# Kernel optimization log

Measured on AMD Instinct MI355X. Metric: run time of the kernel, lower is better.

Reference implementation:

```python
import jax, jax.numpy as jnp
import numpy as np

H = 1024        # hidden_size
NH = 16         # num heads
HD = H // NH    # head dim = 64
B, S = 2, 2048


def _linear_params(key, fan_in, fan_out):
    k1, k2 = jax.random.split(key)
    bound = 1.0 / np.sqrt(fan_in)
    w = jax.random.uniform(k1, (fan_in, fan_out), jnp.float32, -bound, bound)
    b = jax.random.uniform(k2, (fan_out,), jnp.float32, -bound, bound)
    return w, b


def setup_inputs() -> dict:
    key = jax.random.key(0)
    ks = jax.random.split(key, 10)
    hidden_states = jax.random.normal(ks[0], (B, S, H), jnp.float32)
    topic_states = jax.random.normal(ks[1], (B, H), jnp.float32)
    attention_mask = jnp.zeros((B, 1, 1, S), jnp.float32)
    Wq, bq = _linear_params(ks[2], H, H)
    Wk, bk = _linear_params(ks[3], H, H)
    Wv, bv = _linear_params(ks[4], H, H)
    Wtp, btp = _linear_params(ks[5], H, H)
    Wta, bta = _linear_params(ks[6], H, H)
    Wd, bd = _linear_params(ks[7], H, H)
    ln_g = jnp.ones((H,), jnp.float32)
    ln_b = jnp.zeros((H,), jnp.float32)
    return {
        "hidden_states": hidden_states, "topic_states": topic_states,
        "attention_mask": attention_mask,
        "Wq": Wq, "bq": bq, "Wk": Wk, "bk": bk, "Wv": Wv, "bv": bv,
        "Wtp": Wtp, "btp": btp, "Wta": Wta, "bta": bta,
        "Wd": Wd, "bd": bd, "ln_g": ln_g, "ln_b": ln_b,
    }


def reference(hidden_states, topic_states, attention_mask,
              Wq, bq, Wk, bk, Wv, bv, Wtp, btp, Wta, bta, Wd, bd, ln_g, ln_b):
    # topic gating: two linears on [B,H], broadcast over seq
    topic_proj = topic_states @ Wtp + btp
    topic_att = topic_proj @ Wta + bta                     # [B,H]
    gate = jax.nn.sigmoid(topic_att)[:, None, :]           # [B,1,H]

    q = hidden_states @ Wq + bq                            # [B,S,H]
    k = (hidden_states @ Wk + bk) * gate                   # sigmoid-gated keys
    v = hidden_states @ Wv + bv

    def split_heads(x):  # [B,S,H] -> [B,NH,S,HD]
        return x.reshape(B, S, NH, HD).transpose(0, 2, 1, 3)

    qh, kh, vh = split_heads(q), split_heads(k), split_heads(v)

    scores = jnp.einsum('bhqd,bhkd->bhqk', qh, kh) / np.sqrt(HD).astype(np.float32)
    scores = scores + attention_mask                       # additive mask
    probs = jax.nn.softmax(scores, axis=-1)                # dropout = identity (eval)
    ctx = jnp.einsum('bhqk,bhkd->bhqd', probs, vh)
    ctx = ctx.transpose(0, 2, 1, 3).reshape(B, S, H)

    out = ctx @ Wd + bd                                    # dense + (eval) dropout
    x = out + hidden_states                                # residual
    mu = jnp.mean(x, axis=-1, keepdims=True)
    var = jnp.mean(jnp.square(x - mu), axis=-1, keepdims=True)
    return (x - mu) * jax.lax.rsqrt(var + 1e-5) * ln_g + ln_b
```

## Files before the change

### kernel.cpp

```cpp
#include <hip/hip_runtime.h>

typedef unsigned short u16;
typedef unsigned int   u32;
typedef __attribute__((ext_vector_type(4)))  float f32x4;
typedef __attribute__((ext_vector_type(16))) float f32x16;
typedef __attribute__((ext_vector_type(8)))  __bf16 bf16x8;
typedef __attribute__((ext_vector_type(8)))  u16  u16x8;
typedef __attribute__((ext_vector_type(4)))  u16  u16x4;

#define HDIM 1024
#define SEQ  2048
#define NB   2
#define MROWS 4096
#define QSCALE 0.18033688011111793f
#define LOG2E  1.4426950408889634f
#define TOPK 64
#define TOPC 16

__device__ __forceinline__ u16 f2bf(float f) {
  u32 u = __float_as_uint(f);
  u32 r = u + 0x7FFFu + ((u >> 16) & 1u);
  return (u16)(r >> 16);
}

__device__ __forceinline__ u32 pkbf(float a, float b) {
  union { __bf16 h[2]; u32 w; } u;
  u.h[0] = (__bf16)a; u.h[1] = (__bf16)b;
  return u.w;
}

__device__ __forceinline__ void gload_lds16(const void* gp, void* lp) {
  __builtin_amdgcn_global_load_lds(
      (const __attribute__((address_space(1))) void*)gp,
      (__attribute__((address_space(3))) void*)lp, 16, 0, 0);
}

__global__ void wt_bf16_kernel(const float* __restrict__ w0, const float* __restrict__ w1,
                               const float* __restrict__ w2, const float* __restrict__ w3,
                               u16* __restrict__ out) {
  const float* W = (blockIdx.z == 0) ? w0 : (blockIdx.z == 1) ? w1 : (blockIdx.z == 2) ? w2 : w3;
  u16* Wt = out + (size_t)blockIdx.z * HDIM * HDIM;
  __shared__ float t[32][33];
  const int k0 = blockIdx.x * 32, n0 = blockIdx.y * 32;
  const int tx = threadIdx.x, ty = threadIdx.y;
#pragma unroll
  for (int j = 0; j < 32; j += 8)
    t[ty + j][tx] = W[(size_t)(k0 + ty + j) * HDIM + n0 + tx];
  __syncthreads();
#pragma unroll
  for (int j = 0; j < 32; j += 8)
    Wt[(size_t)(n0 + ty + j) * HDIM + k0 + tx] = f2bf(t[tx][ty + j]);
}

__global__ void cvt_bf16_kernel(const float* __restrict__ in, u16* __restrict__ out) {
  const size_t i = (size_t)blockIdx.x * 256 + threadIdx.x;
  f32x4 v = *(const f32x4*)(in + i * 4);
  u16x4 o;
#pragma unroll
  for (int e = 0; e < 4; ++e) o[e] = f2bf(v[e]);
  *(u16x4*)(out + i * 4) = o;
}

__global__ void topic_partial_kernel(const float* __restrict__ in, const float* __restrict__ W,
                                     float* __restrict__ part) {
  const int c = blockIdx.x;
  const int b = blockIdx.y;
  const int t = threadIdx.x;
  const float* inb = in + b * HDIM + c * TOPK;
  f32x4 acc = {};
#pragma unroll 8
  for (int k = 0; k < TOPK; ++k) {
    const f32x4 w4 = *(const f32x4*)(W + (size_t)(c * TOPK + k) * HDIM + t * 4);
    acc += inb[k] * w4;
  }
  *(f32x4*)(part + ((size_t)(b * TOPC + c)) * HDIM + t * 4) = acc;
}

__global__ void topic_reduce_kernel(const float* __restrict__ part, const float* __restrict__ bias,
                                    float* __restrict__ out, int sigmoid_mode) {
  const int b = blockIdx.y;
  const int n = blockIdx.x * 256 + threadIdx.x;
  float s = bias[n];
#pragma unroll
  for (int c = 0; c < TOPC; ++c) s += part[((size_t)(b * TOPC + c)) * HDIM + n];
  out[b * HDIM + n] = sigmoid_mode ? (1.f / (1.f + __expf(-s))) : s;
}

template <int MODE>
__global__ __launch_bounds__(256, 2)
void gemm_kernel(const u16* __restrict__ A, const u16* __restrict__ Wt,
                 const float* __restrict__ b0, const float* __restrict__ b1,
                 const float* __restrict__ b2, const float* __restrict__ gate,
                 const float* __restrict__ resid,
                 u16* __restrict__ outb, float* __restrict__ outf) {
  const int n0 = blockIdx.x * 128;
  const int m0 = blockIdx.y * 128;
  const int z = blockIdx.z;
  const u16* W = Wt + (size_t)z * (HDIM * HDIM);
  const float* bias = (MODE == 0) ? (z == 0 ? b0 : (z == 1 ? b1 : b2)) : b0;

  __shared__ __align__(16) u16 Alds[128 * 64];
  __shared__ __align__(16) u16 Blds[128 * 64];

  const int tid = threadIdx.x;
  const int lane = tid & 63;
  const int w = tid >> 6;
  const int wm = w >> 1, wn = w & 1;
  const int srow = tid >> 3, sslot = tid & 7;

  f32x4 acc[4][4] = {};

  for (int k0 = 0; k0 < HDIM; k0 += 64) {
    __syncthreads();
#pragma unroll
    for (int j = 0; j < 4; ++j) {
      const int row = j * 32 + srow;
      const int gs = (sslot ^ (row & 7)) * 8;
      gload_lds16(A + (size_t)(m0 + row) * HDIM + k0 + gs, Alds + j * 2048 + w * 512);
      gload_lds16(W + (size_t)(n0 + row) * HDIM + k0 + gs, Blds + j * 2048 + w * 512);
    }
    __syncthreads();
#pragma unroll
    for (int kk = 0; kk < 2; ++kk) {
      const int slot = ((((kk << 2) + (lane >> 4)) ^ (lane & 7)) << 3);
      bf16x8 af[4], bfr[4];
#pragma unroll
      for (int i = 0; i < 4; ++i) {
        af[i]  = *(const bf16x8*)(&Alds[(wm * 64 + i * 16 + (lane & 15)) * 64 + slot]);
        bfr[i] = *(const bf16x8*)(&Blds[(wn * 64 + i * 16 + (lane & 15)) * 64 + slot]);
      }
#pragma unroll
      for (int i = 0; i < 4; ++i)
#pragma unroll
        for (int jn = 0; jn < 4; ++jn)
          acc[i][jn] = __builtin_amdgcn_mfma_f32_16x16x32_bf16(af[i], bfr[jn], acc[i][jn], 0, 0, 0);
    }
  }

  const int rbase = (lane >> 4) << 2;
#pragma unroll
  for (int i = 0; i < 4; ++i) {
#pragma unroll
    for (int jn = 0; jn < 4; ++jn) {
      const int n = n0 + wn * 64 + jn * 16 + (lane & 15);
      const float bv = bias[n];
#pragma unroll
      for (int r = 0; r < 4; ++r) {
        const int m = m0 + wm * 64 + i * 16 + rbase + r;
        float v = acc[i][jn][r] + bv;
        if (MODE == 0) {
          if (z == 0) v *= QSCALE;
          if (z == 1) v *= gate[(m >> 11) * HDIM + n];
          outb[(size_t)z * MROWS * HDIM + (size_t)m * HDIM + n] = f2bf(v);
        } else {
          v += resid[(size_t)m * HDIM + n];
          outf[(size_t)m * HDIM + n] = v;
        }
      }
    }
  }
}

__global__ void vtrans_kernel(const u16* __restrict__ v, u16* __restrict__ vt) {
  const int s0 = blockIdx.x * 64, h = blockIdx.y, b = blockIdx.z;
  __shared__ u16 T[64][66];
  const int tid = threadIdx.x;
  const int r = tid >> 3, c8 = (tid & 7) * 8;
#pragma unroll
  for (int p = 0; p < 2; ++p) {
    const int srow = p * 32 + r;
    const u16x8 val = *(const u16x8*)(v + (size_t)(b * SEQ + s0 + srow) * HDIM + h * 64 + c8);
#pragma unroll
    for (int e = 0; e < 8; ++e) T[srow][c8 + e] = val[e];
  }
  __syncthreads();
#pragma unroll
  for (int p = 0; p < 2; ++p) {
    const int drow = p * 32 + r;
    u16x8 o;
#pragma unroll
    for (int e = 0; e < 8; ++e) o[e] = T[c8 + e][drow];
    *(u16x8*)(vt + (size_t)((b * 16 + h) * 64 + drow) * SEQ + s0 + c8) = o;
  }
}

__global__ __launch_bounds__(256, 2)
void attn_kernel(const u16* __restrict__ Q, const u16* __restrict__ K,
                 const u16* __restrict__ Vt, const float* __restrict__ mask,
                 u16* __restrict__ O) {
  const int q0 = blockIdx.x * 128;
  const int h = blockIdx.y;
  const int b = blockIdx.z;
  const size_t base = ((size_t)b * SEQ) * HDIM + h * 64;
  const size_t vtbase = (size_t)((b * 16 + h) * 64) * SEQ;
  const int tid = threadIdx.x, lane = tid & 63, w = tid >> 6;
  const int hh = lane >> 5;
  const int ql = lane & 31;
  const int NT = SEQ / 64;

  __shared__ __align__(16) u16 Kss[2][64 * 64];
  __shared__ __align__(16) u16 Vts[2][64 * 64];

  bf16x8 Qf[4];
  {
    const u16* qp = Q + base + (size_t)(q0 + w * 32 + ql) * HDIM;
#pragma unroll
    for (int ds = 0; ds < 4; ++ds)
      Qf[ds] = *(const bf16x8*)(qp + ds * 16 + hh * 8);
  }

  const int l3 = lane >> 3, l7 = lane & 7;
  const u16* ksrc0 = K + base + (size_t)(w * 8 + l3) * HDIM + ((l7 ^ l3) << 3);
  const u16* ksrc1 = K + base + (size_t)((4 + w) * 8 + l3) * HDIM + ((l7 ^ l3) << 3);
  const u16* vsrc0 = Vt + vtbase + (size_t)(w * 16 + l3) * SEQ + (((l7 ^ l3 ^ (w * 2)) & 7) << 3);
  const u16* vsrc1 = Vt + vtbase + (size_t)(w * 16 + 8 + l3) * SEQ + (((l7 ^ l3 ^ (w * 2 + 1)) & 7) << 3);

  const u16* kaddr[4];
#pragma unroll
  for (int ds = 0; ds < 4; ++ds)
    kaddr[ds] = &Kss[0][ql * 64 + (((ds * 2 + hh) ^ (ql & 7)) << 3)];
  const u16* vaddr[2][4];
#pragma unroll
  for (int dt = 0; dt < 2; ++dt) {
    const int d = dt * 32 + ql;
    const int sw = (d & 7) ^ ((d >> 3) & 7);
#pragma unroll
    for (int c = 0; c < 4; ++c)
      vaddr[dt][c] = &Vts[0][d * 64 + (((c * 2 + hh) ^ sw) << 3)];
  }

  float m_run = -1e30f, l_run = 0.f;
  f32x16 accA = {}, accB = {};

  auto STAGE = [&](int ncur, int t1) {
    const size_t ko = (size_t)(t1 * 64) * HDIM;
    const int vo = t1 * 64;
    gload_lds16(ksrc0 + ko, &Kss[ncur][w * 512]);
    gload_lds16(ksrc1 + ko, &Kss[ncur][(4 + w) * 512]);
    gload_lds16(vsrc0 + vo, &Vts[ncur][w * 1024]);
    gload_lds16(vsrc1 + vo, &Vts[ncur][w * 1024 + 512]);
  };

  STAGE(0, 0);
  __syncthreads();

  auto BODY = [&](int t, const int cur) {
    if (t + 1 < NT) STAGE(cur ^ 1, t + 1);
    const int kvt0 = t * 64;
#pragma unroll
    for (int kvb = 0; kvb < 2; ++kvb) {
      f32x16 sv = {};
#pragma unroll
      for (int ds = 0; ds < 4; ++ds) {
        const bf16x8 kf = *(const bf16x8*)(kaddr[ds] + cur * 4096 + kvb * 2048);
        sv = __builtin_amdgcn_mfma_f32_32x32x16_bf16(kf, Qf[ds], sv, 0, 0, 0);
      }
      f32x4 m4[4];
      {
        const float* mrow = mask + (size_t)b * SEQ + kvt0 + kvb * 32 + hh * 4;
#pragma unroll
        for (int g = 0; g < 4; ++g) m4[g] = *(const f32x4*)(mrow + g * 8);
      }
      f32x16 s_;
#pragma unroll
      for (int j = 0; j < 16; ++j) s_[j] = fmaf(m4[j >> 2][j & 3], LOG2E, sv[j]);

      float mx0 = fmaxf(fmaxf(s_[0], s_[1]), fmaxf(s_[2], s_[3]));
      float mx1 = fmaxf(fmaxf(s_[4], s_[5]), fmaxf(s_[6], s_[7]));
      float mx2 = fmaxf(fmaxf(s_[8], s_[9]), fmaxf(s_[10], s_[11]));
      float mx3 = fmaxf(fmaxf(s_[12], s_[13]), fmaxf(s_[14], s_[15]));
      float mx = fmaxf(fmaxf(mx0, mx1), fmaxf(mx2, mx3));
      mx = fmaxf(mx, __shfl_xor(mx, 32));

      if (!__all(mx <= m_run + 8.f)) {
        const float mnew = fmaxf(m_run, mx);
        const float corr = __builtin_amdgcn_exp2f(m_run - mnew);
        m_run = mnew;
        l_run *= corr;
#pragma unroll
        for (int j = 0; j < 16; ++j) {
          const float cj = __shfl(corr, (j & 3) + 8 * (j >> 2) + 4 * hh);
          accA[j] *= cj; accB[j] *= cj;
        }
      }

      f32x16 p_;
#pragma unroll
      for (int j = 0; j < 16; ++j) p_[j] = __builtin_amdgcn_exp2f(s_[j] - m_run);
      {
        float r0 = (p_[0] + p_[1]) + (p_[2] + p_[3]);
        float r1 = (p_[4] + p_[5]) + (p_[6] + p_[7]);
        float r2 = (p_[8] + p_[9]) + (p_[10] + p_[11]);
        float r3 = (p_[12] + p_[13]) + (p_[14] + p_[15]);
        float rs = (r0 + r1) + (r2 + r3);
        rs += __shfl_xor(rs, 32);
        l_run += rs;
      }

#pragma unroll
      for (int s2 = 0; s2 < 2; ++s2) {
        const u32 a0 = pkbf(p_[s2 * 8 + 0], p_[s2 * 8 + 1]);
        const u32 a1 = pkbf(p_[s2 * 8 + 2], p_[s2 * 8 + 3]);
        const u32 b0v = pkbf(p_[s2 * 8 + 4], p_[s2 * 8 + 5]);
        const u32 b1v = pkbf(p_[s2 * 8 + 6], p_[s2 * 8 + 7]);
        const u32 sd0 = hh ? a0 : b0v, sd1 = hh ? a1 : b1v;
        const u32 r0 = (u32)__shfl_xor((int)sd0, 32);
        const u32 r1 = (u32)__shfl_xor((int)sd1, 32);
        union { u32 u[4]; bf16x8 v; } pu;
        pu.u[0] = hh ? r0 : a0;  pu.u[1] = hh ? r1 : a1;
        pu.u[2] = hh ? b0v : r0; pu.u[3] = hh ? b1v : r1;
        const int c = kvb * 2 + s2;
        const bf16x8 vf0 = *(const bf16x8*)(vaddr[0][c] + cur * 4096);
        const bf16x8 vf1 = *(const bf16x8*)(vaddr[1][c] + cur * 4096);
        accA = __builtin_amdgcn_mfma_f32_32x32x16_bf16(pu.v, vf0, accA, 0, 0, 0);
        accB = __builtin_amdgcn_mfma_f32_32x32x16_bf16(pu.v, vf1, accB, 0, 0, 0);
      }
    }
    __syncthreads();
  };

  for (int tt = 0; tt < NT; tt += 2) {
    BODY(tt, 0);
    BODY(tt + 1, 1);
  }

  const float linv = 1.f / l_run;
#pragma unroll
  for (int j = 0; j < 16; ++j) {
    const int rq = (j & 3) + 8 * (j >> 2) + 4 * hh;
    const float lj = __shfl(linv, rq);
    const size_t orow = base + (size_t)(q0 + w * 32 + rq) * HDIM;
    O[orow + ql]      = f2bf(accA[j] * lj);
    O[orow + 32 + ql] = f2bf(accB[j] * lj);
  }
}

__global__ void ln_kernel(const float* __restrict__ x, const float* __restrict__ g,
                          const float* __restrict__ bb, float* __restrict__ out) {
  const int row = blockIdx.x;
  const int tid = threadIdx.x;
  const f32x4 v = *(const f32x4*)(x + (size_t)row * HDIM + tid * 4);
  float s = v[0] + v[1] + v[2] + v[3];
  float s2 = v[0] * v[0] + v[1] * v[1] + v[2] * v[2] + v[3] * v[3];
#pragma unroll
  for (int o = 1; o < 64; o <<= 1) { s += __shfl_xor(s, o); s2 += __shfl_xor(s2, o); }
  __shared__ float rs[4], rs2[4];
  if ((tid & 63) == 0) { rs[tid >> 6] = s; rs2[tid >> 6] = s2; }
  __syncthreads();
  s = rs[0] + rs[1] + rs[2] + rs[3];
  s2 = rs2[0] + rs2[1] + rs2[2] + rs2[3];
  const float mu = s * (1.f / HDIM);
  const float var = s2 * (1.f / HDIM) - mu * mu;
  const float inv = rsqrtf(var + 1e-5f);
  f32x4 o4;
#pragma unroll
  for (int e = 0; e < 4; ++e) {
    const int c = tid * 4 + e;
    o4[e] = (v[e] - mu) * inv * g[c] + bb[c];
  }
  *(f32x4*)(out + (size_t)row * HDIM + tid * 4) = o4;
}

extern "C" void kernel_launch(void* const* d_in, const int* in_sizes, int n_in,
                              void* d_out, int out_size, void* d_ws, size_t ws_size,
                              hipStream_t stream) {
  const float* hidden = (const float*)d_in[0];
  const float* topic  = (const float*)d_in[1];
  const float* mask   = (const float*)d_in[2];
  const float* Wq  = (const float*)d_in[3];  const float* bq  = (const float*)d_in[4];
  const float* Wk  = (const float*)d_in[5];  const float* bk  = (const float*)d_in[6];
  const float* Wv  = (const float*)d_in[7];  const float* bv  = (const float*)d_in[8];
  const float* Wtp = (const float*)d_in[9];  const float* btp = (const float*)d_in[10];
  const float* Wta = (const float*)d_in[11]; const float* bta = (const float*)d_in[12];
  const float* Wd  = (const float*)d_in[13]; const float* bd  = (const float*)d_in[14];
  const float* lng = (const float*)d_in[15]; const float* lnb = (const float*)d_in[16];
  float* out = (float*)d_out;

  char* ws = (char*)d_ws;
  u16* hs_bf  = (u16*)(ws);
  u16* WtAll  = (u16*)(ws + (size_t)(8u << 20));
  u16* qkv    = (u16*)(ws + (size_t)(16u << 20));
  u16* ctx    = (u16*)(ws + (size_t)(40u << 20));
  u16* VtG    = (u16*)(ws + (size_t)(48u << 20));
  float* xbuf = (float*)(ws + (size_t)(16u << 20));
  float* tproj = (float*)(ws + (size_t)(64u << 20));
  float* tgate = (float*)(ws + (size_t)(64u << 20) + 8192);
  float* tpart = (float*)(ws + (size_t)(16u << 20));

  wt_bf16_kernel<<<dim3(32, 32, 4), dim3(32, 8), 0, stream>>>(Wq, Wk, Wv, Wd, WtAll);
  cvt_bf16_kernel<<<4096, 256, 0, stream>>>(hidden, hs_bf);
  topic_partial_kernel<<<dim3(TOPC, NB), 256, 0, stream>>>(topic, Wtp, tpart);
  topic_reduce_kernel<<<dim3(4, NB), 256, 0, stream>>>(tpart, btp, tproj, 0);
  topic_partial_kernel<<<dim3(TOPC, NB), 256, 0, stream>>>(tproj, Wta, tpart);
  topic_reduce_kernel<<<dim3(4, NB), 256, 0, stream>>>(tpart, bta, tgate, 1);
  gemm_kernel<0><<<dim3(8, 32, 3), 256, 0, stream>>>(hs_bf, WtAll, bq, bk, bv, tgate,
                                                     nullptr, qkv, nullptr);
  vtrans_kernel<<<dim3(32, 16, NB), 256, 0, stream>>>(qkv + 2 * (size_t)MROWS * HDIM, VtG);
  attn_kernel<<<dim3(16, 16, NB), 256, 0, stream>>>(qkv, qkv + (size_t)MROWS * HDIM,
                                                    VtG, mask, ctx);
  gemm_kernel<1><<<dim3(8, 32, 1), 256, 0, stream>>>(ctx, WtAll + 3 * (size_t)HDIM * HDIM,
                                                     bd, nullptr, nullptr, nullptr, hidden,
                                                     nullptr, xbuf);
  ln_kernel<<<4096, 256, 0, stream>>>(xbuf, lng, lnb, out);
}
```

Measured before the change: 166.3 us.

## Load K and V tiles directly from global into registers, dropping LDS staging

Replaces the double-buffered shared-memory staging of K and V tiles (global-to-LDS loads plus barriers) with direct per-lane global loads into registers. K fragments for the next tile are software-prefetched into a second register set while the current tile is computed. This removes LDS traffic and the per-tile __syncthreads. In exchange, each of the four waves now loads K/V redundantly from global/L2, and the extra fragment registers raise VGPR pressure, which may hurt occupancy.

New measurement: 224.4 us. 1.35x slower.

```diff
diff --git a/kernel.cpp b/kernel.cpp
--- a/kernel.cpp
+++ b/kernel.cpp
@@ -192,15 +192,11 @@
   const int h = blockIdx.y;
   const int b = blockIdx.z;
   const size_t base = ((size_t)b * SEQ) * HDIM + h * 64;
-  const size_t vtbase = (size_t)((b * 16 + h) * 64) * SEQ;
   const int tid = threadIdx.x, lane = tid & 63, w = tid >> 6;
   const int hh = lane >> 5;
   const int ql = lane & 31;
   const int NT = SEQ / 64;
 
-  __shared__ __align__(16) u16 Kss[2][64 * 64];
-  __shared__ __align__(16) u16 Vts[2][64 * 64];
-
   bf16x8 Qf[4];
   {
     const u16* qp = Q + base + (size_t)(q0 + w * 32 + ql) * HDIM;
@@ -209,55 +205,48 @@
       Qf[ds] = *(const bf16x8*)(qp + ds * 16 + hh * 8);
   }
 
-  const int l3 = lane >> 3, l7 = lane & 7;
-  const u16* ksrc0 = K + base + (size_t)(w * 8 + l3) * HDIM + ((l7 ^ l3) << 3);
-  const u16* ksrc1 = K + base + (size_t)((4 + w) * 8 + l3) * HDIM + ((l7 ^ l3) << 3);
-  const u16* vsrc0 = Vt + vtbase + (size_t)(w * 16 + l3) * SEQ + (((l7 ^ l3 ^ (w * 2)) & 7) << 3);
-  const u16* vsrc1 = Vt + vtbase + (size_t)(w * 16 + 8 + l3) * SEQ + (((l7 ^ l3 ^ (w * 2 + 1)) & 7) << 3);
-
-  const u16* kaddr[4];
-#pragma unroll
-  for (int ds = 0; ds < 4; ++ds)
-    kaddr[ds] = &Kss[0][ql * 64 + (((ds * 2 + hh) ^ (ql & 7)) << 3)];
-  const u16* vaddr[2][4];
-#pragma unroll
-  for (int dt = 0; dt < 2; ++dt) {
-    const int d = dt * 32 + ql;
-    const int sw = (d & 7) ^ ((d >> 3) & 7);
-#pragma unroll
-    for (int c = 0; c < 4; ++c)
-      vaddr[dt][c] = &Vts[0][d * 64 + (((c * 2 + hh) ^ sw) << 3)];
-  }
+  const u16* Kp = K + base + (size_t)ql * HDIM + hh * 8;
+  const u16* Vp = Vt + (size_t)((b * 16 + h) * 64 + ql) * SEQ + hh * 8;
+  const float* mrow_base = mask + (size_t)b * SEQ + hh * 4;
 
   float m_run = -1e30f, l_run = 0.f;
   f32x16 accA = {}, accB = {};
 
-  auto STAGE = [&](int ncur, int t1) {
-    const size_t ko = (size_t)(t1 * 64) * HDIM;
-    const int vo = t1 * 64;
-    gload_lds16(ksrc0 + ko, &Kss[ncur][w * 512]);
-    gload_lds16(ksrc1 + ko, &Kss[ncur][(4 + w) * 512]);
-    gload_lds16(vsrc0 + vo, &Vts[ncur][w * 1024]);
-    gload_lds16(vsrc1 + vo, &Vts[ncur][w * 1024 + 512]);
-  };
-
-  STAGE(0, 0);
-  __syncthreads();
-
-  auto BODY = [&](int t, const int cur) {
-    if (t + 1 < NT) STAGE(cur ^ 1, t + 1);
+  bf16x8 kfA[2][4], kfB[2][4], vf[2][4];
+
+#define LOADK(KF, T_)                                                          \
+  {                                                                            \
+    const u16* kp_ = Kp + (size_t)((T_) * 64) * HDIM;                          \
+    _Pragma("unroll")                                                          \
+    for (int kvb = 0; kvb < 2; ++kvb)                                          \
+      _Pragma("unroll")                                                        \
+      for (int ds = 0; ds < 4; ++ds)                                           \
+        KF[kvb][ds] = *(const bf16x8*)(kp_ + (size_t)(kvb * 32) * HDIM + ds * 16); \
+  }
+#define LOADV(T_)                                                              \
+  {                                                                            \
+    const u16* vp_ = Vp + (T_) * 64;                                           \
+    _Pragma("unroll")                                                          \
+    for (int dt = 0; dt < 2; ++dt)                                             \
+      _Pragma("unroll")                                                        \
+      for (int c = 0; c < 4; ++c)                                              \
+        vf[dt][c] = *(const bf16x8*)(vp_ + (size_t)(dt * 32) * SEQ + c * 16);  \
+  }
+
+  LOADK(kfA, 0);
+
+  auto COMPUTE = [&](int t, const bf16x8 (&kf)[2][4]) {
     const int kvt0 = t * 64;
 #pragma unroll
     for (int kvb = 0; kvb < 2; ++kvb) {
       f32x16 sv = {};
 #pragma unroll
-      for (int ds = 0; ds < 4; ++ds) {
-        const bf16x8 kf = *(const bf16x8*)(kaddr[ds] + cur * 4096 + kvb * 2048);
-        sv = __builtin_amdgcn_mfma_f32_32x32x16_bf16(kf, Qf[ds], sv, 0, 0, 0);
-      }
+      for (int ds = 0; ds < 4; ++ds)
+        sv = __builtin_amdgcn_mfma_f32_32x32x16_bf16(kf[kvb][ds], Qf[ds], sv, 0, 0, 0);
+
       f32x4 m4[4];
       {
-        const float* mrow = mask + (size_t)b * SEQ + kvt0 + kvb * 32 + hh * 4;
+        const float* mrow = mrow_base + kvt0 + kvb * 32;
 #pragma unroll
         for (int g = 0; g < 4; ++g) m4[g] = *(const f32x4*)(mrow + g * 8);
       }
@@ -310,19 +299,22 @@
         pu.u[0] = hh ? r0 : a0;  pu.u[1] = hh ? r1 : a1;
         pu.u[2] = hh ? b0v : r0; pu.u[3] = hh ? b1v : r1;
         const int c = kvb * 2 + s2;
-        const bf16x8 vf0 = *(const bf16x8*)(vaddr[0][c] + cur * 4096);
-        const bf16x8 vf1 = *(const bf16x8*)(vaddr[1][c] + cur * 4096);
-        accA = __builtin_amdgcn_mfma_f32_32x32x16_bf16(pu.v, vf0, accA, 0, 0, 0);
-        accB = __builtin_amdgcn_mfma_f32_32x32x16_bf16(pu.v, vf1, accB, 0, 0, 0);
+        accA = __builtin_amdgcn_mfma_f32_32x32x16_bf16(pu.v, vf[0][c], accA, 0, 0, 0);
+        accB = __builtin_amdgcn_mfma_f32_32x32x16_bf16(pu.v, vf[1][c], accB, 0, 0, 0);
       }
     }
-    __syncthreads();
   };
 
   for (int tt = 0; tt < NT; tt += 2) {
-    BODY(tt, 0);
-    BODY(tt + 1, 1);
-  }
+    LOADV(tt);
+    LOADK(kfB, tt + 1);
+    COMPUTE(tt, kfA);
+    LOADV(tt + 1);
+    if (tt + 2 < NT) LOADK(kfA, tt + 2);
+    COMPUTE(tt + 1, kfB);
+  }
+#undef LOADK
+#undef LOADV
 
   const float linv = 1.f / l_run;
 #pragma unroll
```

## Software-pipeline attention QK and PV stages; fuse V transpose into QKV GEMM

Applied to the files above, without the earlier changes.

The attention loop is restructured so the QK^T MFMAs and softmax for tile t+1 are computed while the PV MFMAs for tile t run, with K and V staged separately into LDS at different points to overlap loads with compute. Separately, the V projection epilogue of the QKV GEMM now writes V directly in transposed head-major layout, which removes the standalone vtrans kernel and its extra global round trip. The pipelining raises register pressure (two score tiles plus packed probability fragments) and the transposed epilogue writes are narrower and strided.

After: 156.8 us. -5.7%, faster.

```diff
diff --git a/kernel.cpp b/kernel.cpp
--- a/kernel.cpp
+++ b/kernel.cpp
@@ -92,7 +92,7 @@
                  const float* __restrict__ b0, const float* __restrict__ b1,
                  const float* __restrict__ b2, const float* __restrict__ gate,
                  const float* __restrict__ resid,
-                 u16* __restrict__ outb, float* __restrict__ outf) {
+                 u16* __restrict__ outb, u16* __restrict__ outv, float* __restrict__ outf) {
   const int n0 = blockIdx.x * 128;
   const int m0 = blockIdx.y * 128;
   const int z = blockIdx.z;
@@ -138,6 +138,22 @@
   }
 
   const int rbase = (lane >> 4) << 2;
+  if (MODE == 0 && z == 2) {
+#pragma unroll
+    for (int i = 0; i < 4; ++i) {
+#pragma unroll
+      for (int jn = 0; jn < 4; ++jn) {
+        const int n = n0 + wn * 64 + jn * 16 + (lane & 15);
+        const float bv = bias[n];
+        const int m = m0 + wm * 64 + i * 16 + rbase;
+        u16x4 o;
+#pragma unroll
+        for (int r = 0; r < 4; ++r) o[r] = f2bf(acc[i][jn][r] + bv);
+        *(u16x4*)(outv + ((size_t)((m >> 11) * 16 + (n >> 6)) * 64 + (n & 63)) * SEQ + (m & 2047)) = o;
+      }
+    }
+    return;
+  }
 #pragma unroll
   for (int i = 0; i < 4; ++i) {
 #pragma unroll
@@ -158,29 +174,6 @@
         }
       }
     }
-  }
-}
-
-__global__ void vtrans_kernel(const u16* __restrict__ v, u16* __restrict__ vt) {
-  const int s0 = blockIdx.x * 64, h = blockIdx.y, b = blockIdx.z;
-  __shared__ u16 T[64][66];
-  const int tid = threadIdx.x;
-  const int r = tid >> 3, c8 = (tid & 7) * 8;
-#pragma unroll
-  for (int p = 0; p < 2; ++p) {
-    const int srow = p * 32 + r;
-    const u16x8 val = *(const u16x8*)(v + (size_t)(b * SEQ + s0 + srow) * HDIM + h * 64 + c8);
-#pragma unroll
-    for (int e = 0; e < 8; ++e) T[srow][c8 + e] = val[e];
-  }
-  __syncthreads();
-#pragma unroll
-  for (int p = 0; p < 2; ++p) {
-    const int drow = p * 32 + r;
-    u16x8 o;
-#pragma unroll
-    for (int e = 0; e < 8; ++e) o[e] = T[c8 + e][drow];
-    *(u16x8*)(vt + (size_t)((b * 16 + h) * 64 + drow) * SEQ + s0 + c8) = o;
   }
 }
 
@@ -229,99 +222,139 @@
       vaddr[dt][c] = &Vts[0][d * 64 + (((c * 2 + hh) ^ sw) << 3)];
   }
 
+  const float* mrow_base = mask + (size_t)b * SEQ + hh * 4;
+
   float m_run = -1e30f, l_run = 0.f;
   f32x16 accA = {}, accB = {};
-
-  auto STAGE = [&](int ncur, int t1) {
+  bf16x8 pfA[4], pfB[4];
+
+  auto STAGEK = [&](const int buf, const int t1) {
     const size_t ko = (size_t)(t1 * 64) * HDIM;
+    gload_lds16(ksrc0 + ko, &Kss[buf][w * 512]);
+    gload_lds16(ksrc1 + ko, &Kss[buf][(4 + w) * 512]);
+  };
+  auto STAGEV = [&](const int buf, const int t1) {
     const int vo = t1 * 64;
-    gload_lds16(ksrc0 + ko, &Kss[ncur][w * 512]);
-    gload_lds16(ksrc1 + ko, &Kss[ncur][(4 + w) * 512]);
-    gload_lds16(vsrc0 + vo, &Vts[ncur][w * 1024]);
-    gload_lds16(vsrc1 + vo, &Vts[ncur][w * 1024 + 512]);
-  };
-
-  STAGE(0, 0);
-  __syncthreads();
-
-  auto BODY = [&](int t, const int cur) {
-    if (t + 1 < NT) STAGE(cur ^ 1, t + 1);
-    const int kvt0 = t * 64;
+    gload_lds16(vsrc0 + vo, &Vts[buf][w * 1024]);
+    gload_lds16(vsrc1 + vo, &Vts[buf][w * 1024 + 512]);
+  };
+
+  auto EXPPACK = [&](const f32x16& s0_, const f32x16& s1_, bf16x8 (&pfout)[4]) {
+    f32x16 p0_, p1_;
+#pragma unroll
+    for (int j = 0; j < 16; ++j) {
+      p0_[j] = __builtin_amdgcn_exp2f(s0_[j] - m_run);
+      p1_[j] = __builtin_amdgcn_exp2f(s1_[j] - m_run);
+    }
+    float r8[8];
+#pragma unroll
+    for (int j = 0; j < 8; ++j)
+      r8[j] = (p0_[j] + p0_[j + 8]) + (p1_[j] + p1_[j + 8]);
+    float rs = ((r8[0] + r8[1]) + (r8[2] + r8[3])) + ((r8[4] + r8[5]) + (r8[6] + r8[7]));
+    rs += __shfl_xor(rs, 32);
+    l_run += rs;
 #pragma unroll
     for (int kvb = 0; kvb < 2; ++kvb) {
-      f32x16 sv = {};
-#pragma unroll
-      for (int ds = 0; ds < 4; ++ds) {
-        const bf16x8 kf = *(const bf16x8*)(kaddr[ds] + cur * 4096 + kvb * 2048);
-        sv = __builtin_amdgcn_mfma_f32_32x32x16_bf16(kf, Qf[ds], sv, 0, 0, 0);
-      }
-      f32x4 m4[4];
-      {
-        const float* mrow = mask + (size_t)b * SEQ + kvt0 + kvb * 32 + hh * 4;
-#pragma unroll
-        for (int g = 0; g < 4; ++g) m4[g] = *(const f32x4*)(mrow + g * 8);
-      }
-      f32x16 s_;
-#pragma unroll
-      for (int j = 0; j < 16; ++j) s_[j] = fmaf(m4[j >> 2][j & 3], LOG2E, sv[j]);
-
-      float mx0 = fmaxf(fmaxf(s_[0], s_[1]), fmaxf(s_[2], s_[3]));
-      float mx1 = fmaxf(fmaxf(s_[4], s_[5]), fmaxf(s_[6], s_[7]));
-      float mx2 = fmaxf(fmaxf(s_[8], s_[9]), fmaxf(s_[10], s_[11]));
-      float mx3 = fmaxf(fmaxf(s_[12], s_[13]), fmaxf(s_[14], s_[15]));
-      float mx = fmaxf(fmaxf(mx0, mx1), fmaxf(mx2, mx3));
-      mx = fmaxf(mx, __shfl_xor(mx, 32));
-
-      if (!__all(mx <= m_run + 8.f)) {
-        const float mnew = fmaxf(m_run, mx);
-        const float corr = __builtin_amdgcn_exp2f(m_run - mnew);
-        m_run = mnew;
-        l_run *= corr;
-#pragma unroll
-        for (int j = 0; j < 16; ++j) {
-          const float cj = __shfl(corr, (j & 3) + 8 * (j >> 2) + 4 * hh);
-          accA[j] *= cj; accB[j] *= cj;
-        }
-      }
-
-      f32x16 p_;
-#pragma unroll
-      for (int j = 0; j < 16; ++j) p_[j] = __builtin_amdgcn_exp2f(s_[j] - m_run);
-      {
-        float r0 = (p_[0] + p_[1]) + (p_[2] + p_[3]);
-        float r1 = (p_[4] + p_[5]) + (p_[6] + p_[7]);
-        float r2 = (p_[8] + p_[9]) + (p_[10] + p_[11]);
-        float r3 = (p_[12] + p_[13]) + (p_[14] + p_[15]);
-        float rs = (r0 + r1) + (r2 + r3);
-        rs += __shfl_xor(rs, 32);
-        l_run += rs;
-      }
-
+      const f32x16& pp = kvb ? p1_ : p0_;
 #pragma unroll
       for (int s2 = 0; s2 < 2; ++s2) {
-        const u32 a0 = pkbf(p_[s2 * 8 + 0], p_[s2 * 8 + 1]);
-        const u32 a1 = pkbf(p_[s2 * 8 + 2], p_[s2 * 8 + 3]);
-        const u32 b0v = pkbf(p_[s2 * 8 + 4], p_[s2 * 8 + 5]);
-        const u32 b1v = pkbf(p_[s2 * 8 + 6], p_[s2 * 8 + 7]);
+        const u32 a0 = pkbf(pp[s2 * 8 + 0], pp[s2 * 8 + 1]);
+        const u32 a1 = pkbf(pp[s2 * 8 + 2], pp[s2 * 8 + 3]);
+        const u32 b0v = pkbf(pp[s2 * 8 + 4], pp[s2 * 8 + 5]);
+        const u32 b1v = pkbf(pp[s2 * 8 + 6], pp[s2 * 8 + 7]);
         const u32 sd0 = hh ? a0 : b0v, sd1 = hh ? a1 : b1v;
         const u32 r0 = (u32)__shfl_xor((int)sd0, 32);
         const u32 r1 = (u32)__shfl_xor((int)sd1, 32);
         union { u32 u[4]; bf16x8 v; } pu;
         pu.u[0] = hh ? r0 : a0;  pu.u[1] = hh ? r1 : a1;
         pu.u[2] = hh ? b0v : r0; pu.u[3] = hh ? b1v : r1;
-        const int c = kvb * 2 + s2;
-        const bf16x8 vf0 = *(const bf16x8*)(vaddr[0][c] + cur * 4096);
-        const bf16x8 vf1 = *(const bf16x8*)(vaddr[1][c] + cur * 4096);
-        accA = __builtin_amdgcn_mfma_f32_32x32x16_bf16(pu.v, vf0, accA, 0, 0, 0);
-        accB = __builtin_amdgcn_mfma_f32_32x32x16_bf16(pu.v, vf1, accB, 0, 0, 0);
+        pfout[kvb * 2 + s2] = pu.v;
       }
     }
+  };
+
+  auto RESCALE = [&](const float mx) {
+    const float mnew = fmaxf(m_run, mx);
+    const float corr = __builtin_amdgcn_exp2f(m_run - mnew);
+    m_run = mnew; l_run *= corr;
+#pragma unroll
+    for (int j = 0; j < 16; ++j) {
+      const float cj = __shfl(corr, (j & 3) + 8 * (j >> 2) + 4 * hh);
+      accA[j] *= cj; accB[j] *= cj;
+    }
+  };
+
+  auto QKMM = [&](const int tq, const int kb, f32x16& s0_, f32x16& s1_, float& mx) {
+    f32x16 sv0 = {}, sv1 = {};
+#pragma unroll
+    for (int ds = 0; ds < 4; ++ds) {
+      const bf16x8 kf0 = *(const bf16x8*)(kaddr[ds] + kb * 4096);
+      const bf16x8 kf1 = *(const bf16x8*)(kaddr[ds] + kb * 4096 + 2048);
+      sv0 = __builtin_amdgcn_mfma_f32_32x32x16_bf16(kf0, Qf[ds], sv0, 0, 0, 0);
+      sv1 = __builtin_amdgcn_mfma_f32_32x32x16_bf16(kf1, Qf[ds], sv1, 0, 0, 0);
+    }
+    f32x4 m40[4], m41[4];
+    const float* mrow = mrow_base + tq * 64;
+#pragma unroll
+    for (int g = 0; g < 4; ++g) {
+      m40[g] = *(const f32x4*)(mrow + g * 8);
+      m41[g] = *(const f32x4*)(mrow + 32 + g * 8);
+    }
+#pragma unroll
+    for (int j = 0; j < 16; ++j) {
+      s0_[j] = fmaf(m40[j >> 2][j & 3], LOG2E, sv0[j]);
+      s1_[j] = fmaf(m41[j >> 2][j & 3], LOG2E, sv1[j]);
+    }
+    float t8[8];
+#pragma unroll
+    for (int j = 0; j < 8; ++j)
+      t8[j] = fmaxf(fmaxf(s0_[j], s0_[j + 8]), fmaxf(s1_[j], s1_[j + 8]));
+    mx = fmaxf(fmaxf(fmaxf(t8[0], t8[1]), fmaxf(t8[2], t8[3])),
+               fmaxf(fmaxf(t8[4], t8[5]), fmaxf(t8[6], t8[7])));
+    mx = fmaxf(mx, __shfl_xor(mx, 32));
+  };
+
+  STAGEK(0, 0); STAGEV(0, 0);
+  __syncthreads();
+  STAGEK(1, 1); STAGEV(1, 1);
+  {
+    f32x16 s0_, s1_; float mx;
+    QKMM(0, 0, s0_, s1_, mx);
+    if (!__all(mx <= m_run + 8.f)) RESCALE(mx);
+    EXPPACK(s0_, s1_, pfA);
+  }
+  __syncthreads();
+
+  auto STEP = [&](const int t, const int X, const bf16x8 (&pfin)[4], bf16x8 (&pfout)[4]) {
+    if (t + 2 < NT) STAGEK(X, t + 2);
+    f32x16 s0_, s1_; float mx;
+    QKMM(t + 1, X ^ 1, s0_, s1_, mx);
+    const bool resc = !__all(mx <= m_run + 8.f);
+#pragma unroll
+    for (int c = 0; c < 4; ++c) {
+      const bf16x8 vf0 = *(const bf16x8*)(vaddr[0][c] + X * 4096);
+      const bf16x8 vf1 = *(const bf16x8*)(vaddr[1][c] + X * 4096);
+      accA = __builtin_amdgcn_mfma_f32_32x32x16_bf16(pfin[c], vf0, accA, 0, 0, 0);
+      accB = __builtin_amdgcn_mfma_f32_32x32x16_bf16(pfin[c], vf1, accB, 0, 0, 0);
+    }
+    if (resc) RESCALE(mx);
+    EXPPACK(s0_, s1_, pfout);
     __syncthreads();
-  };
-
-  for (int tt = 0; tt < NT; tt += 2) {
-    BODY(tt, 0);
-    BODY(tt + 1, 1);
+    if (t + 2 < NT) STAGEV(X, t + 2);
+  };
+
+  for (int t = 0; t < NT - 2; t += 2) {
+    STEP(t, 0, pfA, pfB);
+    STEP(t + 1, 1, pfB, pfA);
+  }
+  STEP(NT - 2, 0, pfA, pfB);
+
+#pragma unroll
+  for (int c = 0; c < 4; ++c) {
+    const bf16x8 vf0 = *(const bf16x8*)(vaddr[0][c] + 4096);
+    const bf16x8 vf1 = *(const bf16x8*)(vaddr[1][c] + 4096);
+    accA = __builtin_amdgcn_mfma_f32_32x32x16_bf16(pfB[c], vf0, accA, 0, 0, 0);
+    accB = __builtin_amdgcn_mfma_f32_32x32x16_bf16(pfB[c], vf1, accB, 0, 0, 0);
   }
 
   const float linv = 1.f / l_run;
@@ -394,12 +427,11 @@
   topic_partial_kernel<<<dim3(TOPC, NB), 256, 0, stream>>>(tproj, Wta, tpart);
   topic_reduce_kernel<<<dim3(4, NB), 256, 0, stream>>>(tpart, bta, tgate, 1);
   gemm_kernel<0><<<dim3(8, 32, 3), 256, 0, stream>>>(hs_bf, WtAll, bq, bk, bv, tgate,
-                                                     nullptr, qkv, nullptr);
-  vtrans_kernel<<<dim3(32, 16, NB), 256, 0, stream>>>(qkv + 2 * (size_t)MROWS * HDIM, VtG);
+                                                     nullptr, qkv, VtG, nullptr);
   attn_kernel<<<dim3(16, 16, NB), 256, 0, stream>>>(qkv, qkv + (size_t)MROWS * HDIM,
                                                     VtG, mask, ctx);
   gemm_kernel<1><<<dim3(8, 32, 1), 256, 0, stream>>>(ctx, WtAll + 3 * (size_t)HDIM * HDIM,
                                                      bd, nullptr, nullptr, nullptr, hidden,
-                                                     nullptr, xbuf);
+                                                     nullptr, nullptr, xbuf);
   ln_kernel<<<4096, 256, 0, stream>>>(xbuf, lng, lnb, out);
 }
```
